# Kernel optimization log

Measured on AMD Instinct MI355X. Metric: run time of the kernel, lower is better.

Reference implementation:

```python
import jax, jax.numpy as jnp
import numpy as np

E = 1_000_000      # number of edges
T = 2_000_000      # number of angle triplets
EDGE_DIM = 64
HIDDEN = 128
LN_EPS = 1e-5


def _layer_norm(x, gamma, beta):
    mu = jnp.mean(x, axis=-1, keepdims=True)
    var = jnp.mean(jnp.square(x - mu), axis=-1, keepdims=True)
    return (x - mu) * jax.lax.rsqrt(var + LN_EPS) * gamma + beta


def setup_inputs() -> dict:
    key = jax.random.key(0)
    ks = jax.random.split(key, 8)
    in_dim = 2 * EDGE_DIM + 4  # 132

    def lin(k, fan_in, fan_out):
        bound = 1.0 / np.sqrt(fan_in)
        kw, kb = jax.random.split(k)
        W = jax.random.uniform(kw, (fan_in, fan_out), jnp.float32, -bound, bound)
        b = jax.random.uniform(kb, (fan_out,), jnp.float32, -bound, bound)
        return W, b

    W1, b1 = lin(ks[0], in_dim, HIDDEN)
    W2, b2 = lin(ks[1], HIDDEN, HIDDEN)
    W3, b3 = lin(ks[2], HIDDEN, EDGE_DIM)

    return {
        "edge_feat": jax.random.normal(ks[3], (E, EDGE_DIM), jnp.float32),
        "triplet_idx": jax.random.randint(ks[4], (T, 2), 0, E, jnp.int64) if jax.config.jax_enable_x64 else jax.random.randint(ks[4], (T, 2), 0, E, jnp.int32),
        "triplet_geo": jax.random.uniform(ks[5], (T, 4), jnp.float32),
        "W1": W1, "b1": b1,
        "g1": jnp.ones((HIDDEN,), jnp.float32), "be1": jnp.zeros((HIDDEN,), jnp.float32),
        "W2": W2, "b2": b2,
        "g2": jnp.ones((HIDDEN,), jnp.float32), "be2": jnp.zeros((HIDDEN,), jnp.float32),
        "W3": W3, "b3": b3,
        "gn": jnp.ones((EDGE_DIM,), jnp.float32), "bn": jnp.zeros((EDGE_DIM,), jnp.float32),
    }


def reference(edge_feat, triplet_idx, triplet_geo,
              W1, b1, g1, be1, W2, b2, g2, be2, W3, b3, gn, bn):
    num_edges = edge_feat.shape[0]
    e_ij = triplet_idx[:, 0]
    e_kj = triplet_idx[:, 1]

    f_ij = edge_feat[e_ij]                      # [T, edge_dim] gather
    f_kj = edge_feat[e_kj]                      # [T, edge_dim] gather
    x = jnp.concatenate([f_ij, f_kj, triplet_geo], axis=1)  # [T, 2*edge_dim+4]

    # mlp_phi: Linear -> SiLU -> LayerNorm -> Linear -> SiLU -> LayerNorm
    h = _layer_norm(jax.nn.silu(x @ W1 + b1), g1, be1)
    m = _layer_norm(jax.nn.silu(h @ W2 + b2), g2, be2)  # [T, hidden]

    # scatter-mean over e_ij with dim_size = num_edges
    sums = jax.ops.segment_sum(m, e_ij, num_segments=num_edges)
    cnts = jax.ops.segment_sum(jnp.ones((m.shape[0],), m.dtype), e_ij, num_segments=num_edges)
    agg = sums / jnp.maximum(cnts, 1.0)[:, None]         # [E, hidden]

    out = edge_feat + (agg @ W3 + b3)
    return _layer_norm(out, gn, bn)
```

## Files before the change

### kernel.cpp

```cpp
#include <hip/hip_runtime.h>
#include <hip/hip_bf16.h>
#include <stdint.h>

typedef __attribute__((ext_vector_type(8))) short short8;
typedef __attribute__((ext_vector_type(4))) float f32x4;
typedef unsigned short u16;

#define OFF_PSUM 0ULL
#define OFF_CNT  256000000ULL
#define OFF_EBF  260000000ULL
#define OFF_WT1  388000000ULL
#define OFF_WT2  (OFF_WT1 + 40960ULL)
#define OFF_WP3  (OFF_WT2 + 32768ULL)
#define OFF_S2   (OFF_WP3 + 16384ULL)
#define OFF_C2   (OFF_S2 + 512ULL)
#define OFF_S3   (OFF_C2 + 512ULL)
#define OFF_T3   (OFF_S3 + 256ULL)

#define LDS_H   40960
#define LDS_P1S 73728
#define LDS_P1Q 74752
#define LDS_P2S 75776
#define LDS_P2Q 76800
#define LDS_EIJ 77824
#define LDS_EKJ 78336
#define LDS_TOTAL 78848

__device__ __forceinline__ u16 f2bf(float f) {
  union { float f; uint32_t u; } c; c.f = f;
  uint32_t u = c.u;
  return (u16)((u + 0x7FFFu + ((u >> 16) & 1u)) >> 16);
}
__device__ __forceinline__ uint32_t pkbf(float lo, float hi) {
  float2 t; t.x = lo; t.y = hi;
  __hip_bfloat162 h = __float22bfloat162_rn(t);
  uint32_t u; __builtin_memcpy(&u, &h, 4);
  return u;
}
__device__ __forceinline__ float silu(float y) {
  return y * __builtin_amdgcn_rcpf(1.0f + __expf(-y));
}

#define MFMA16(a, b, c) __builtin_amdgcn_mfma_f32_16x16x32_bf16((a), (b), (c), 0, 0, 0)


__global__ __launch_bounds__(256) void k_conv_edge(const float* __restrict__ ef,
                                                   u16* __restrict__ ebf) {
  int i = blockIdx.x * 256 + threadIdx.x;
  float4 v = ((const float4*)ef)[i];
  ushort4 o;
  o.x = f2bf(v.x); o.y = f2bf(v.y); o.z = f2bf(v.z); o.w = f2bf(v.w);
  ((ushort4*)ebf)[i] = o;
}

__global__ __launch_bounds__(256) void k_pack_w(const float* __restrict__ W1,
                                                const float* __restrict__ W2,
                                                const float* __restrict__ W3,
                                                const float* __restrict__ g1,
                                                const float* __restrict__ g2,
                                                u16* __restrict__ wt1,
                                                u16* __restrict__ wt2,
                                                u16* __restrict__ wp3) {
  int i = blockIdx.x * 256 + threadIdx.x;
  if (i < 20480) {
    int n = i / 160, k = i - n * 160;
    wt1[i] = (k < 132) ? f2bf(W1[k * 128 + n]) : (u16)0;
  } else if (i < 36864) {
    int i2 = i - 20480;
    int n = i2 >> 7, k = i2 & 127;
    wt2[i2] = f2bf(g1[k] * W2[k * 128 + n]);
  } else if (i < 45056) {
    int i3 = i - 36864;
    int j = i3 & 7, n = (i3 >> 3) & 63, kb = i3 >> 9;
    int k = kb * 8 + j;
    wp3[i3] = f2bf(g2[k] * W3[k * 64 + n]);
  }
}

__global__ __launch_bounds__(256) void k_pack_vec(
    const float* __restrict__ W2, const float* __restrict__ W3,
    const float* __restrict__ g1, const float* __restrict__ be1, const float* __restrict__ b2,
    const float* __restrict__ g2, const float* __restrict__ be2,
    float* __restrict__ s2, float* __restrict__ c2,
    float* __restrict__ s3, float* __restrict__ t3) {
  int t = threadIdx.x;
  if (t < 128) {
    float a = 0.f, b = 0.f;
    for (int k = 0; k < 128; ++k) {
      float w = W2[k * 128 + t];
      a += g1[k] * w; b += be1[k] * w;
    }
    s2[t] = a; c2[t] = b + b2[t];
  } else if (t < 192) {
    int n = t - 128;
    float a = 0.f, b = 0.f;
    for (int k = 0; k < 128; ++k) {
      float w = W3[k * 64 + n];
      a += g2[k] * w; b += be2[k] * w;
    }
    s3[n] = a; t3[n] = b;
  }
}


__global__ __launch_bounds__(512, 4) void k_triplet(
    const u16* __restrict__ ebf, const int* __restrict__ tidx,
    const float* __restrict__ geo,
    const u16* __restrict__ wt1, const u16* __restrict__ wt2, const u16* __restrict__ wp3,
    const float* __restrict__ b1,
    const float* __restrict__ s2v, const float* __restrict__ c2v,
    const float* __restrict__ s3v,
    float* __restrict__ psum, float* __restrict__ cnt) {
  extern __shared__ char smem[];
  float* P1S = (float*)(smem + LDS_P1S);
  float* P1Q = (float*)(smem + LDS_P1Q);
  float* P2S = (float*)(smem + LDS_P2S);
  float* P2Q = (float*)(smem + LDS_P2Q);
  int* EIJ = (int*)(smem + LDS_EIJ);
  int* EKJ = (int*)(smem + LDS_EKJ);

  const int tid = threadIdx.x;
  const int wave = tid >> 6, lane = tid & 63;
  const int wm = wave >> 2, wn = wave & 3;
  const int l15 = lane & 15, lg = lane >> 4;
  const int t0 = blockIdx.x * 128;

  if (tid < 128) {
    int2 p = ((const int2*)tidx)[t0 + tid];
    EIJ[tid] = p.x; EKJ[tid] = p.y;
    atomicAdd(&cnt[p.x], 1.0f);
  }
  __syncthreads();

  {
    const int r = tid >> 2, s = tid & 3;
    const int e = (s < 2) ? EIJ[r] : EKJ[r];
    const uint4* src = (const uint4*)(ebf + (size_t)e * 64) + (s & 1) * 4;
    uint4 v0 = src[0], v1 = src[1], v2 = src[2], v3 = src[3];
    const int swz = (r & 7) << 4;
    char* rowp = smem + r * 320;
    *(uint4*)(rowp + ((s * 64 + 0) ^ swz)) = v0;
    *(uint4*)(rowp + ((s * 64 + 16) ^ swz)) = v1;
    *(uint4*)(rowp + ((s * 64 + 32) ^ swz)) = v2;
    *(uint4*)(rowp + ((s * 64 + 48) ^ swz)) = v3;
    const int tswz = (r & 3) << 4;
    if (s == 0) {
      float4 gq = ((const float4*)geo)[t0 + r];
      uint2 gw;
      gw.x = pkbf(gq.x, gq.y); gw.y = pkbf(gq.z, gq.w);
      char* tp = rowp + 256 + (0 ^ tswz);
      *(uint2*)tp = gw;
      *(uint2*)(tp + 8) = (uint2){0, 0};
    } else {
      *(uint4*)(rowp + 256 + ((s * 16) ^ tswz)) = (uint4){0, 0, 0, 0};
    }
  }
  __syncthreads();

  f32x4 acc[4][2];
#pragma unroll
  for (int mf = 0; mf < 4; ++mf) { acc[mf][0] = (f32x4)0.f; acc[mf][1] = (f32x4)0.f; }
  const short8* w1p = (const short8*)wt1;
#pragma unroll
  for (int s5 = 0; s5 < 5; ++s5) {
    short8 aw[4], bx[2];
#pragma unroll
    for (int mf = 0; mf < 4; ++mf)
      aw[mf] = w1p[(wm * 64 + mf * 16 + l15) * 20 + s5 * 4 + lg];
#pragma unroll
    for (int f = 0; f < 2; ++f) {
      int trip = wn * 32 + f * 16 + l15;
      int off;
      if (s5 < 4) off = (s5 * 64 + lg * 16) ^ ((trip & 7) << 4);
      else off = 256 + ((lg * 16) ^ ((trip & 3) << 4));
      bx[f] = *(const short8*)(smem + trip * 320 + off);
    }
#pragma unroll
    for (int mf = 0; mf < 4; ++mf) {
      acc[mf][0] = MFMA16(aw[mf], bx[0], acc[mf][0]);
      acc[mf][1] = MFMA16(aw[mf], bx[1], acc[mf][1]);
    }
  }

  {
    float4 b1f[4];
#pragma unroll
    for (int mf = 0; mf < 4; ++mf)
      b1f[mf] = *(const float4*)(b1 + wm * 64 + mf * 16 + lg * 4);
    float st[2] = {0.f, 0.f}, sq[2] = {0.f, 0.f};
#pragma unroll
    for (int mf = 0; mf < 4; ++mf)
#pragma unroll
      for (int f = 0; f < 2; ++f)
#pragma unroll
        for (int q = 0; q < 4; ++q) {
          float v = silu(acc[mf][f][q] + b1f[mf][q]);
          acc[mf][f][q] = v;
          st[f] += v; sq[f] += v * v;
        }
#pragma unroll
    for (int f = 0; f < 2; ++f) {
      st[f] += __shfl_xor(st[f], 16); sq[f] += __shfl_xor(sq[f], 16);
      st[f] += __shfl_xor(st[f], 32); sq[f] += __shfl_xor(sq[f], 32);
    }
    if (lg == 0) {
#pragma unroll
      for (int f = 0; f < 2; ++f) {
        int trip = wn * 32 + f * 16 + l15;
        P1S[trip * 2 + wm] = st[f];
        P1Q[trip * 2 + wm] = sq[f];
      }
    }
#pragma unroll
    for (int mf = 0; mf < 4; ++mf)
#pragma unroll
      for (int f = 0; f < 2; ++f) {
        int trip = wn * 32 + f * 16 + l15;
        uint2 w;
        w.x = pkbf(acc[mf][f][0], acc[mf][f][1]);
        w.y = pkbf(acc[mf][f][2], acc[mf][f][3]);
        *(uint2*)(smem + LDS_H + trip * 256 +
                  ((wm * 128 + mf * 32 + lg * 8) ^ ((trip & 7) << 4))) = w;
      }
  }
  __syncthreads();

#pragma unroll
  for (int mf = 0; mf < 4; ++mf) { acc[mf][0] = (f32x4)0.f; acc[mf][1] = (f32x4)0.f; }
  const short8* w2p = (const short8*)wt2;
#pragma unroll
  for (int s4 = 0; s4 < 4; ++s4) {
    short8 aw[4], bx[2];
#pragma unroll
    for (int mf = 0; mf < 4; ++mf)
      aw[mf] = w2p[(wm * 64 + mf * 16 + l15) * 16 + s4 * 4 + lg];
#pragma unroll
    for (int f = 0; f < 2; ++f) {
      int trip = wn * 32 + f * 16 + l15;
      bx[f] = *(const short8*)(smem + LDS_H + trip * 256 +
                               ((s4 * 64 + lg * 16) ^ ((trip & 7) << 4)));
    }
#pragma unroll
    for (int mf = 0; mf < 4; ++mf) {
      acc[mf][0] = MFMA16(aw[mf], bx[0], acc[mf][0]);
      acc[mf][1] = MFMA16(aw[mf], bx[1], acc[mf][1]);
    }
  }

  {
    float4 s2f[4], c2f[4];
#pragma unroll
    for (int mf = 0; mf < 4; ++mf) {
      s2f[mf] = *(const float4*)(s2v + wm * 64 + mf * 16 + lg * 4);
      c2f[mf] = *(const float4*)(c2v + wm * 64 + mf * 16 + lg * 4);
    }
    float mu[2], inv[2];
#pragma unroll
    for (int f = 0; f < 2; ++f) {
      int trip = wn * 32 + f * 16 + l15;
      float sm = P1S[trip * 2] + P1S[trip * 2 + 1];
      float qq = P1Q[trip * 2] + P1Q[trip * 2 + 1];
      mu[f] = sm * 0.0078125f;
      inv[f] = rsqrtf(fmaxf(qq * 0.0078125f - mu[f] * mu[f], 0.f) + 1e-5f);
    }
    float st[2] = {0.f, 0.f}, sq[2] = {0.f, 0.f};
#pragma unroll
    for (int mf = 0; mf < 4; ++mf)
#pragma unroll
      for (int f = 0; f < 2; ++f)
#pragma unroll
        for (int q = 0; q < 4; ++q) {
          float y = inv[f] * (acc[mf][f][q] - mu[f] * s2f[mf][q]) + c2f[mf][q];
          float v = silu(y);
          acc[mf][f][q] = v;
          st[f] += v; sq[f] += v * v;
        }
#pragma unroll
    for (int f = 0; f < 2; ++f) {
      st[f] += __shfl_xor(st[f], 16); sq[f] += __shfl_xor(sq[f], 16);
      st[f] += __shfl_xor(st[f], 32); sq[f] += __shfl_xor(sq[f], 32);
    }
    if (lg == 0) {
#pragma unroll
      for (int f = 0; f < 2; ++f) {
        int trip = wn * 32 + f * 16 + l15;
        P2S[trip * 2 + wm] = st[f];
        P2Q[trip * 2 + wm] = sq[f];
      }
    }
#pragma unroll
    for (int mf = 0; mf < 4; ++mf)
#pragma unroll
      for (int f = 0; f < 2; ++f) {
        int trip = wn * 32 + f * 16 + l15;
        uint2 w;
        w.x = pkbf(acc[mf][f][0], acc[mf][f][1]);
        w.y = pkbf(acc[mf][f][2], acc[mf][f][3]);
        *(uint2*)(smem + trip * 256 +
                  ((wm * 128 + mf * 32 + lg * 8) ^ ((trip & 7) << 4))) = w;
      }
  }

  const short8* wb3 = (const short8*)wp3;
  const int n3 = wn * 16 + l15;
  short8 w3f[4];
#pragma unroll
  for (int s4 = 0; s4 < 4; ++s4) w3f[s4] = wb3[(s4 * 4 + lg) * 64 + n3];
  float s3c = s3v[n3];

  __syncthreads();

  f32x4 acc3[4];
#pragma unroll
  for (int mf = 0; mf < 4; ++mf) acc3[mf] = (f32x4)0.f;
#pragma unroll
  for (int s4 = 0; s4 < 4; ++s4) {
    short8 a[4];
#pragma unroll
    for (int mf = 0; mf < 4; ++mf) {
      int row = wm * 64 + mf * 16 + l15;
      a[mf] = *(const short8*)(smem + row * 256 +
                               ((s4 * 64 + lg * 16) ^ ((row & 7) << 4)));
    }
#pragma unroll
    for (int mf = 0; mf < 4; ++mf) acc3[mf] = MFMA16(a[mf], w3f[s4], acc3[mf]);
  }

#pragma unroll
  for (int mf = 0; mf < 4; ++mf)
#pragma unroll
    for (int q = 0; q < 4; ++q) {
      int row = wm * 64 + mf * 16 + lg * 4 + q;
      float sm = P2S[row * 2] + P2S[row * 2 + 1];
      float qq = P2Q[row * 2] + P2Q[row * 2 + 1];
      float mu = sm * 0.0078125f;
      float inv = rsqrtf(fmaxf(qq * 0.0078125f - mu * mu, 0.f) + 1e-5f);
      float y = inv * (acc3[mf][q] - mu * s3c);
      int e = EIJ[row];
      atomicAdd(psum + (size_t)e * 64 + n3, y);
    }
}


__global__ __launch_bounds__(256) void k_final(
    const float* __restrict__ psum, const float* __restrict__ cnt,
    const float* __restrict__ ef, const float* __restrict__ b3,
    const float* __restrict__ t3, const float* __restrict__ gn,
    const float* __restrict__ bn, float* __restrict__ out) {
  int g = blockIdx.x * 256 + threadIdx.x;
  int e = g >> 2, s = g & 3;
  float cv = cnt[e];
  float ic = 1.0f / fmaxf(cv, 1.0f);
  float tw = (cv > 0.f) ? 1.0f : 0.0f;
  float x[16];
  const float4* ps = (const float4*)(psum + (size_t)e * 64 + s * 16);
  const float4* fe = (const float4*)(ef + (size_t)e * 64 + s * 16);
  const float4* p3 = (const float4*)(b3 + s * 16);
  const float4* pt = (const float4*)(t3 + s * 16);
#pragma unroll
  for (int i = 0; i < 4; ++i) {
    float4 a = ps[i], b = fe[i], c = p3[i], d = pt[i];
    x[4 * i + 0] = b.x + a.x * ic + c.x + tw * d.x;
    x[4 * i + 1] = b.y + a.y * ic + c.y + tw * d.y;
    x[4 * i + 2] = b.z + a.z * ic + c.z + tw * d.z;
    x[4 * i + 3] = b.w + a.w * ic + c.w + tw * d.w;
  }
  float sum = 0.f, ss = 0.f;
#pragma unroll
  for (int i = 0; i < 16; ++i) { sum += x[i]; ss += x[i] * x[i]; }
  sum += __shfl_xor(sum, 1); ss += __shfl_xor(ss, 1);
  sum += __shfl_xor(sum, 2); ss += __shfl_xor(ss, 2);
  float mu = sum * (1.0f / 64.0f);
  float inv = rsqrtf(ss * (1.0f / 64.0f) - mu * mu + 1e-5f);
  float4* po = (float4*)(out + (size_t)e * 64 + s * 16);
#pragma unroll
  for (int i = 0; i < 4; ++i) {
    float4 gv = ((const float4*)(gn + s * 16))[i];
    float4 bv = ((const float4*)(bn + s * 16))[i];
    float4 o;
    o.x = (x[4 * i + 0] - mu) * inv * gv.x + bv.x;
    o.y = (x[4 * i + 1] - mu) * inv * gv.y + bv.y;
    o.z = (x[4 * i + 2] - mu) * inv * gv.z + bv.z;
    o.w = (x[4 * i + 3] - mu) * inv * gv.w + bv.w;
    po[i] = o;
  }
}

extern "C" void kernel_launch(void* const* d_in, const int* in_sizes, int n_in,
                              void* d_out, int out_size, void* d_ws, size_t ws_size,
                              hipStream_t stream) {
  const float* edge_feat = (const float*)d_in[0];
  const int* tidx = (const int*)d_in[1];
  const float* geo = (const float*)d_in[2];
  const float* W1 = (const float*)d_in[3];
  const float* b1 = (const float*)d_in[4];
  const float* g1 = (const float*)d_in[5];
  const float* be1 = (const float*)d_in[6];
  const float* W2 = (const float*)d_in[7];
  const float* b2 = (const float*)d_in[8];
  const float* g2 = (const float*)d_in[9];
  const float* be2 = (const float*)d_in[10];
  const float* W3 = (const float*)d_in[11];
  const float* b3 = (const float*)d_in[12];
  const float* gn = (const float*)d_in[13];
  const float* bn = (const float*)d_in[14];

  char* ws = (char*)d_ws;
  float* psum = (float*)(ws + OFF_PSUM);
  float* cnt = (float*)(ws + OFF_CNT);
  u16* ebf = (u16*)(ws + OFF_EBF);
  u16* wt1 = (u16*)(ws + OFF_WT1);
  u16* wt2 = (u16*)(ws + OFF_WT2);
  u16* wp3 = (u16*)(ws + OFF_WP3);
  float* s2 = (float*)(ws + OFF_S2);
  float* c2 = (float*)(ws + OFF_C2);
  float* s3 = (float*)(ws + OFF_S3);
  float* t3 = (float*)(ws + OFF_T3);
  float* out = (float*)d_out;

  hipMemsetAsync(ws, 0, 260000000ULL, stream);
  k_conv_edge<<<62500, 256, 0, stream>>>(edge_feat, ebf);
  k_pack_w<<<176, 256, 0, stream>>>(W1, W2, W3, g1, g2, wt1, wt2, wp3);
  k_pack_vec<<<1, 256, 0, stream>>>(W2, W3, g1, be1, b2, g2, be2, s2, c2, s3, t3);

  hipFuncSetAttribute((const void*)k_triplet,
                      hipFuncAttributeMaxDynamicSharedMemorySize, LDS_TOTAL);
  k_triplet<<<15625, 512, LDS_TOTAL, stream>>>(ebf, tidx, geo, wt1, wt2, wp3,
                                               b1, s2, c2, s3, psum, cnt);
  k_final<<<15625, 256, 0, stream>>>(psum, cnt, edge_feat, b3, t3, gn, bn, out);
}
```

Before: 1.148 ms.

## Shrink triplet tile to 64 and gather edge features straight into registers

Each k_triplet block now handles 64 triplets with 256 threads instead of 128 with 512. Gathered edge features are loaded from global memory directly into MFMA B-operand registers instead of being staged in shared memory. LDS use drops from about 77KB to about 22KB, which removes one staging barrier and is meant to let more blocks reside per CU, helping hide the latency of the random gather. The third matmul is remapped so each wave covers 16 rows across all 64 outputs, which changes the order of the scatter atomics. In exchange, register pressure rises from holding eight gathered fragments across the first GEMM, and weight loads are amortised over fewer triplets.

```diff
diff --git a/kernel.cpp b/kernel.cpp
--- a/kernel.cpp
+++ b/kernel.cpp
@@ -17,14 +17,14 @@
 #define OFF_S3   (OFF_C2 + 512ULL)
 #define OFF_T3   (OFF_S3 + 256ULL)
 
-#define LDS_H   40960
-#define LDS_P1S 73728
-#define LDS_P1Q 74752
-#define LDS_P2S 75776
-#define LDS_P2Q 76800
-#define LDS_EIJ 77824
-#define LDS_EKJ 78336
-#define LDS_TOTAL 78848
+#define LDS_HM   0
+#define LDS_TAIL 16384
+#define LDS_P1S  20480
+#define LDS_P1Q  20992
+#define LDS_P2S  21504
+#define LDS_P2Q  22016
+#define LDS_EIJ  22528
+#define LDS_TOTAL 22784
 
 __device__ __forceinline__ u16 f2bf(float f) {
   union { float f; uint32_t u; } c; c.f = f;
@@ -103,7 +103,7 @@
 }
 
 
-__global__ __launch_bounds__(512, 4) void k_triplet(
+__global__ __launch_bounds__(256, 5) void k_triplet(
     const u16* __restrict__ ebf, const int* __restrict__ tidx,
     const float* __restrict__ geo,
     const u16* __restrict__ wt1, const u16* __restrict__ wt2, const u16* __restrict__ wp3,
@@ -111,51 +111,52 @@
     const float* __restrict__ s2v, const float* __restrict__ c2v,
     const float* __restrict__ s3v,
     float* __restrict__ psum, float* __restrict__ cnt) {
-  extern __shared__ char smem[];
+  __shared__ __align__(16) char smem[LDS_TOTAL];
   float* P1S = (float*)(smem + LDS_P1S);
   float* P1Q = (float*)(smem + LDS_P1Q);
   float* P2S = (float*)(smem + LDS_P2S);
   float* P2Q = (float*)(smem + LDS_P2Q);
   int* EIJ = (int*)(smem + LDS_EIJ);
-  int* EKJ = (int*)(smem + LDS_EKJ);
 
   const int tid = threadIdx.x;
   const int wave = tid >> 6, lane = tid & 63;
-  const int wm = wave >> 2, wn = wave & 3;
+  const int wm = wave >> 1, wn = wave & 1;
   const int l15 = lane & 15, lg = lane >> 4;
-  const int t0 = blockIdx.x * 128;
-
-  if (tid < 128) {
+  const int t0 = blockIdx.x * 64;
+
+  const int tA = wn * 32 + l15;
+  const int tB = tA + 16;
+  int2 pA = ((const int2*)tidx)[t0 + tA];
+  int2 pB = ((const int2*)tidx)[t0 + tB];
+
+  const short8* eb = (const short8*)ebf;
+  short8 bxA0 = eb[(size_t)pA.x * 8 + lg];
+  short8 bxA1 = eb[(size_t)pA.x * 8 + 4 + lg];
+  short8 bxA2 = eb[(size_t)pA.y * 8 + lg];
+  short8 bxA3 = eb[(size_t)pA.y * 8 + 4 + lg];
+  short8 bxB0 = eb[(size_t)pB.x * 8 + lg];
+  short8 bxB1 = eb[(size_t)pB.x * 8 + 4 + lg];
+  short8 bxB2 = eb[(size_t)pB.y * 8 + lg];
+  short8 bxB3 = eb[(size_t)pB.y * 8 + 4 + lg];
+
+  if (tid < 64) {
     int2 p = ((const int2*)tidx)[t0 + tid];
-    EIJ[tid] = p.x; EKJ[tid] = p.y;
+    EIJ[tid] = p.x;
     atomicAdd(&cnt[p.x], 1.0f);
+    float4 gq = ((const float4*)geo)[t0 + tid];
+    uint2 gw; gw.x = pkbf(gq.x, gq.y); gw.y = pkbf(gq.z, gq.w);
+    char* tp = smem + LDS_TAIL + tid * 64;
+    const int ts = (tid & 3) << 4;
+    *(uint2*)(tp + (0 ^ ts)) = gw;
+    *(uint2*)(tp + (0 ^ ts) + 8) = (uint2){0, 0};
+    *(uint4*)(tp + (16 ^ ts)) = (uint4){0, 0, 0, 0};
+    *(uint4*)(tp + (32 ^ ts)) = (uint4){0, 0, 0, 0};
+    *(uint4*)(tp + (48 ^ ts)) = (uint4){0, 0, 0, 0};
   }
   __syncthreads();
 
-  {
-    const int r = tid >> 2, s = tid & 3;
-    const int e = (s < 2) ? EIJ[r] : EKJ[r];
-    const uint4* src = (const uint4*)(ebf + (size_t)e * 64) + (s & 1) * 4;
-    uint4 v0 = src[0], v1 = src[1], v2 = src[2], v3 = src[3];
-    const int swz = (r & 7) << 4;
-    char* rowp = smem + r * 320;
-    *(uint4*)(rowp + ((s * 64 + 0) ^ swz)) = v0;
-    *(uint4*)(rowp + ((s * 64 + 16) ^ swz)) = v1;
-    *(uint4*)(rowp + ((s * 64 + 32) ^ swz)) = v2;
-    *(uint4*)(rowp + ((s * 64 + 48) ^ swz)) = v3;
-    const int tswz = (r & 3) << 4;
-    if (s == 0) {
-      float4 gq = ((const float4*)geo)[t0 + r];
-      uint2 gw;
-      gw.x = pkbf(gq.x, gq.y); gw.y = pkbf(gq.z, gq.w);
-      char* tp = rowp + 256 + (0 ^ tswz);
-      *(uint2*)tp = gw;
-      *(uint2*)(tp + 8) = (uint2){0, 0};
-    } else {
-      *(uint4*)(rowp + 256 + ((s * 16) ^ tswz)) = (uint4){0, 0, 0, 0};
-    }
-  }
-  __syncthreads();
+  short8 btA = *(const short8*)(smem + LDS_TAIL + tA * 64 + ((lg * 16) ^ ((tA & 3) << 4)));
+  short8 btB = *(const short8*)(smem + LDS_TAIL + tB * 64 + ((lg * 16) ^ ((tB & 3) << 4)));
 
   f32x4 acc[4][2];
 #pragma unroll
@@ -163,22 +164,17 @@
   const short8* w1p = (const short8*)wt1;
 #pragma unroll
   for (int s5 = 0; s5 < 5; ++s5) {
-    short8 aw[4], bx[2];
-#pragma unroll
-    for (int mf = 0; mf < 4; ++mf)
-      aw[mf] = w1p[(wm * 64 + mf * 16 + l15) * 20 + s5 * 4 + lg];
-#pragma unroll
-    for (int f = 0; f < 2; ++f) {
-      int trip = wn * 32 + f * 16 + l15;
-      int off;
-      if (s5 < 4) off = (s5 * 64 + lg * 16) ^ ((trip & 7) << 4);
-      else off = 256 + ((lg * 16) ^ ((trip & 3) << 4));
-      bx[f] = *(const short8*)(smem + trip * 320 + off);
-    }
+    short8 b0, b1x;
+    if (s5 == 0) { b0 = bxA0; b1x = bxB0; }
+    else if (s5 == 1) { b0 = bxA1; b1x = bxB1; }
+    else if (s5 == 2) { b0 = bxA2; b1x = bxB2; }
+    else if (s5 == 3) { b0 = bxA3; b1x = bxB3; }
+    else { b0 = btA; b1x = btB; }
 #pragma unroll
     for (int mf = 0; mf < 4; ++mf) {
-      acc[mf][0] = MFMA16(aw[mf], bx[0], acc[mf][0]);
-      acc[mf][1] = MFMA16(aw[mf], bx[1], acc[mf][1]);
+      short8 aw = w1p[(wm * 64 + mf * 16 + l15) * 20 + s5 * 4 + lg];
+      acc[mf][0] = MFMA16(aw, b0, acc[mf][0]);
+      acc[mf][1] = MFMA16(aw, b1x, acc[mf][1]);
     }
   }
 
@@ -219,7 +215,7 @@
         uint2 w;
         w.x = pkbf(acc[mf][f][0], acc[mf][f][1]);
         w.y = pkbf(acc[mf][f][2], acc[mf][f][3]);
-        *(uint2*)(smem + LDS_H + trip * 256 +
+        *(uint2*)(smem + LDS_HM + trip * 256 +
                   ((wm * 128 + mf * 32 + lg * 8) ^ ((trip & 7) << 4))) = w;
       }
   }
@@ -230,20 +226,20 @@
   const short8* w2p = (const short8*)wt2;
 #pragma unroll
   for (int s4 = 0; s4 < 4; ++s4) {
-    short8 aw[4], bx[2];
-#pragma unroll
-    for (int mf = 0; mf < 4; ++mf)
-      aw[mf] = w2p[(wm * 64 + mf * 16 + l15) * 16 + s4 * 4 + lg];
-#pragma unroll
-    for (int f = 0; f < 2; ++f) {
-      int trip = wn * 32 + f * 16 + l15;
-      bx[f] = *(const short8*)(smem + LDS_H + trip * 256 +
-                               ((s4 * 64 + lg * 16) ^ ((trip & 7) << 4)));
+    short8 bx0, bx1;
+    {
+      int trip = wn * 32 + l15;
+      bx0 = *(const short8*)(smem + LDS_HM + trip * 256 +
+                             ((s4 * 64 + lg * 16) ^ ((trip & 7) << 4)));
+      int trip2 = trip + 16;
+      bx1 = *(const short8*)(smem + LDS_HM + trip2 * 256 +
+                             ((s4 * 64 + lg * 16) ^ ((trip2 & 7) << 4)));
     }
 #pragma unroll
     for (int mf = 0; mf < 4; ++mf) {
-      acc[mf][0] = MFMA16(aw[mf], bx[0], acc[mf][0]);
-      acc[mf][1] = MFMA16(aw[mf], bx[1], acc[mf][1]);
+      short8 aw = w2p[(wm * 64 + mf * 16 + l15) * 16 + s4 * 4 + lg];
+      acc[mf][0] = MFMA16(aw, bx0, acc[mf][0]);
+      acc[mf][1] = MFMA16(aw, bx1, acc[mf][1]);
     }
   }
 
@@ -288,57 +284,56 @@
         P2Q[trip * 2 + wm] = sq[f];
       }
     }
-#pragma unroll
-    for (int mf = 0; mf < 4; ++mf)
-#pragma unroll
-      for (int f = 0; f < 2; ++f) {
-        int trip = wn * 32 + f * 16 + l15;
-        uint2 w;
-        w.x = pkbf(acc[mf][f][0], acc[mf][f][1]);
-        w.y = pkbf(acc[mf][f][2], acc[mf][f][3]);
-        *(uint2*)(smem + trip * 256 +
-                  ((wm * 128 + mf * 32 + lg * 8) ^ ((trip & 7) << 4))) = w;
-      }
-  }
-
+  }
+  __syncthreads();
+
+#pragma unroll
+  for (int mf = 0; mf < 4; ++mf)
+#pragma unroll
+    for (int f = 0; f < 2; ++f) {
+      int trip = wn * 32 + f * 16 + l15;
+      uint2 w;
+      w.x = pkbf(acc[mf][f][0], acc[mf][f][1]);
+      w.y = pkbf(acc[mf][f][2], acc[mf][f][3]);
+      *(uint2*)(smem + LDS_HM + trip * 256 +
+                ((wm * 128 + mf * 32 + lg * 8) ^ ((trip & 7) << 4))) = w;
+    }
+  __syncthreads();
+
+  f32x4 acc3[4];
+#pragma unroll
+  for (int nf = 0; nf < 4; ++nf) acc3[nf] = (f32x4)0.f;
   const short8* wb3 = (const short8*)wp3;
-  const int n3 = wn * 16 + l15;
-  short8 w3f[4];
-#pragma unroll
-  for (int s4 = 0; s4 < 4; ++s4) w3f[s4] = wb3[(s4 * 4 + lg) * 64 + n3];
-  float s3c = s3v[n3];
-
-  __syncthreads();
-
-  f32x4 acc3[4];
-#pragma unroll
-  for (int mf = 0; mf < 4; ++mf) acc3[mf] = (f32x4)0.f;
 #pragma unroll
   for (int s4 = 0; s4 < 4; ++s4) {
-    short8 a[4];
-#pragma unroll
-    for (int mf = 0; mf < 4; ++mf) {
-      int row = wm * 64 + mf * 16 + l15;
-      a[mf] = *(const short8*)(smem + row * 256 +
-                               ((s4 * 64 + lg * 16) ^ ((row & 7) << 4)));
-    }
-#pragma unroll
-    for (int mf = 0; mf < 4; ++mf) acc3[mf] = MFMA16(a[mf], w3f[s4], acc3[mf]);
-  }
-
-#pragma unroll
-  for (int mf = 0; mf < 4; ++mf)
+    int row = wave * 16 + l15;
+    short8 a = *(const short8*)(smem + LDS_HM + row * 256 +
+                                ((s4 * 64 + lg * 16) ^ ((row & 7) << 4)));
+#pragma unroll
+    for (int nf = 0; nf < 4; ++nf) {
+      short8 b = wb3[(s4 * 4 + lg) * 64 + nf * 16 + l15];
+      acc3[nf] = MFMA16(a, b, acc3[nf]);
+    }
+  }
+  {
+    float s3c[4];
+#pragma unroll
+    for (int nf = 0; nf < 4; ++nf) s3c[nf] = s3v[nf * 16 + l15];
 #pragma unroll
     for (int q = 0; q < 4; ++q) {
-      int row = wm * 64 + mf * 16 + lg * 4 + q;
+      int row = wave * 16 + lg * 4 + q;
       float sm = P2S[row * 2] + P2S[row * 2 + 1];
       float qq = P2Q[row * 2] + P2Q[row * 2 + 1];
       float mu = sm * 0.0078125f;
       float inv = rsqrtf(fmaxf(qq * 0.0078125f - mu * mu, 0.f) + 1e-5f);
-      float y = inv * (acc3[mf][q] - mu * s3c);
-      int e = EIJ[row];
-      atomicAdd(psum + (size_t)e * 64 + n3, y);
-    }
+      float* base = psum + (size_t)EIJ[row] * 64;
+#pragma unroll
+      for (int nf = 0; nf < 4; ++nf) {
+        float y = inv * (acc3[nf][q] - mu * s3c[nf]);
+        atomicAdd(base + nf * 16 + l15, y);
+      }
+    }
+  }
 }
 
 
@@ -423,9 +418,7 @@
   k_pack_w<<<176, 256, 0, stream>>>(W1, W2, W3, g1, g2, wt1, wt2, wp3);
   k_pack_vec<<<1, 256, 0, stream>>>(W2, W3, g1, be1, b2, g2, be2, s2, c2, s3, t3);
 
-  hipFuncSetAttribute((const void*)k_triplet,
-                      hipFuncAttributeMaxDynamicSharedMemorySize, LDS_TOTAL);
-  k_triplet<<<15625, 512, LDS_TOTAL, stream>>>(ebf, tidx, geo, wt1, wt2, wp3,
-                                               b1, s2, c2, s3, psum, cnt);
+  k_triplet<<<31250, 256, 0, stream>>>(ebf, tidx, geo, wt1, wt2, wp3,
+                                       b1, s2, c2, s3, psum, cnt);
   k_final<<<15625, 256, 0, stream>>>(psum, cnt, edge_feat, b3, t3, gn, bn, out);
 }
```

New measurement: 1.063 ms. 7.4% less time.
